# Performance work log

Measured on AMD Instinct MI355X. Metric: run time of the kernel, lower is better.

Reference implementation:

```python
import jax, jax.numpy as jnp
import numpy as np

# Constants matching init_kwargs
FEATURE_DIM = 512
QK_DIM = 128
GATE_VALUE = 0.2
TOPK = 32
TEMP = QK_DIM ** (-0.5)


def _l2norm(x, eps=1e-12):
    # F.normalize(p=2, dim=-1): x / max(||x||_2, eps)
    return x / jnp.maximum(jnp.linalg.norm(x, axis=-1, keepdims=True), eps)


def setup_inputs() -> dict:
    key = jax.random.key(0)
    ks = jax.random.split(key, 6)
    B, Nq, Nk = 64, 512, 2048  # Nq == FEATURE_DIM (required by the gather/residual shapes)
    query = jax.random.normal(ks[0], (B, Nq, FEATURE_DIM), dtype=jnp.float32)
    key_feat = jax.random.normal(ks[1], (B, Nk, FEATURE_DIM // 2), dtype=jnp.float32)
    value = jax.random.normal(ks[2], (B, Nk, FEATURE_DIM // 2), dtype=jnp.float32)
    # torch.nn.Linear weights are [out, in]; init N(0, sqrt(2/out_features))
    WQ = jax.random.normal(ks[3], (QK_DIM, FEATURE_DIM), dtype=jnp.float32) * np.sqrt(2.0 / QK_DIM).astype(np.float32)
    WK = jax.random.normal(ks[4], (QK_DIM, FEATURE_DIM // 2), dtype=jnp.float32) * np.sqrt(2.0 / QK_DIM).astype(np.float32)
    WV = jax.random.normal(ks[5], (FEATURE_DIM, FEATURE_DIM // 2), dtype=jnp.float32) * np.sqrt(2.0 / FEATURE_DIM).astype(np.float32)
    return {"query": query, "key_feat": key_feat, "value": value, "WQ": WQ, "WK": WK, "WV": WV}


def reference(query, key_feat, value, WQ, WK, WV):
    # Projections (Linear, no bias) + L2 normalize
    w_q = _l2norm(jnp.einsum('bqf,df->bqd', query, WQ))        # [B, Nq, Dqk]
    w_k = _l2norm(jnp.einsum('bkf,df->bkd', key_feat, WK))     # [B, Nk, Dqk]
    dot_prod = jnp.einsum('bqd,bkd->bqk', w_q, w_k)            # [B, Nq, Nk]
    mask = jnp.max(dot_prod, axis=2) > GATE_VALUE              # [B, Nq] bool
    affinity = jax.nn.softmax(dot_prod * TEMP, axis=-1)        # [B, Nq, Nk]
    topk_vals, topk_idx = jax.lax.top_k(affinity, TOPK)        # [B, Nq, TOPK]
    w_v = _l2norm(jnp.einsum('bkf,cf->bkc', value, WV))        # [B, Nk, F]
    # Faithful torch.gather semantics: index permuted to [B, TOPK, Nq];
    # sel[b,t,c] = w_v[b, topk_idx[b,c,t], c]  (per-channel gather, needs Nq == F)
    sel = jnp.take_along_axis(w_v, jnp.swapaxes(topk_idx, 1, 2), axis=1)  # [B, TOPK, F]
    gather = jnp.einsum('bqt,btc->bqc', topk_vals, sel)        # [B, Nq, F]
    return gather * mask[:, :, None].astype(gather.dtype) + query
```

## Files before the change

### kernel.cpp

```cpp
#include <hip/hip_runtime.h>
#include <math.h>

#define NB   64
#define NQ   512
#define NK   2048
#define FD   512
#define FH   256
#define DQ   128
#define KTOP 32
#define GATEV 0.2f
#define TEMPF 0.08838834764831843f
#define GATEY 0.017677669529663688f

typedef __attribute__((ext_vector_type(8))) short bf16x8;
typedef __attribute__((ext_vector_type(4))) float f32x4;

__device__ __forceinline__ unsigned short f32_bf16_rne(float f) {
    unsigned u = __float_as_uint(f);
    u += 0x7FFFu + ((u >> 16) & 1u);
    return (unsigned short)(u >> 16);
}
__device__ __forceinline__ float exp_small(float y) {
    return 1.f + y * (1.f + y * (0.5f + y * (0.16666667f + y * 0.041666668f)));
}
__device__ __forceinline__ unsigned f32_ordkey(float y, unsigned idc) {
    unsigned bits = __float_as_uint(y);
    unsigned msk = (unsigned)((int)bits >> 31) | 0x80000000u;
    return ((bits ^ msk) & 0xFFFFF800u) | idc;
}
__device__ __forceinline__ float keyval_f(unsigned key) {
    unsigned x = key & 0xFFFFF800u;
    unsigned bits = (x & 0x80000000u) ? (x ^ 0x80000000u) : ~x;
    return __uint_as_float(bits);
}
__device__ __forceinline__ bf16x8 cvt8(const float* p) {
    float4 a = ((const float4*)p)[0];
    float4 b = ((const float4*)p)[1];
    bf16x8 o;
    o[0] = (short)f32_bf16_rne(a.x); o[1] = (short)f32_bf16_rne(a.y);
    o[2] = (short)f32_bf16_rne(a.z); o[3] = (short)f32_bf16_rne(a.w);
    o[4] = (short)f32_bf16_rne(b.x); o[5] = (short)f32_bf16_rne(b.y);
    o[6] = (short)f32_bf16_rne(b.z); o[7] = (short)f32_bf16_rne(b.w);
    return o;
}
__device__ __forceinline__ unsigned umaxu(unsigned a, unsigned b) { return a > b ? a : b; }
__device__ __forceinline__ unsigned uminu(unsigned a, unsigned b) { return a < b ? a : b; }

__global__ __launch_bounds__(256) void kW_cvt(const float* __restrict__ WQ,
                                              const float* __restrict__ WK,
                                              const float* __restrict__ WV,
                                              unsigned short* __restrict__ wqW,
                                              unsigned short* __restrict__ wkW,
                                              unsigned short* __restrict__ wvb) {
    const int i = blockIdx.x * 256 + threadIdx.x;
    if (i < 65536) wqW[i] = f32_bf16_rne(WQ[i]);
    else if (i < 98304) wkW[i - 65536] = f32_bf16_rne(WK[i - 65536]);
    else wvb[i - 98304] = f32_bf16_rne(WV[i - 98304]);
}

__global__ __launch_bounds__(256) void kProjQ(const float* __restrict__ X,
                                              const unsigned short* __restrict__ Wb,
                                              unsigned short* __restrict__ outb) {
    __shared__ __attribute__((aligned(16))) unsigned short wchunk[64 * 512];
    const int tid = threadIdx.x, wave = tid >> 6, lane = tid & 63;
    const int rt = lane & 15, kg = lane >> 4;
    const size_t rowbase = (size_t)blockIdx.x * 64 + wave * 16;
    const float* xrow = X + (rowbase + rt) * 512;
    bf16x8 afr[16];
#pragma unroll
    for (int s = 0; s < 16; ++s) afr[s] = cvt8(xrow + kg * 8 + s * 32);
    f32x4 acc[8];
#pragma unroll
    for (int j = 0; j < 8; ++j) acc[j] = (f32x4){0.f, 0.f, 0.f, 0.f};
#pragma unroll
    for (int ch = 0; ch < 2; ++ch) {
        __syncthreads();
#pragma unroll
        for (int it = 0; it < 16; ++it) {
            int idx = it * 256 + tid;
            int cl = idx >> 6, g = idx & 63;
            *(bf16x8*)(wchunk + (cl * 64 + (g ^ (cl & 7))) * 8) =
                *(const bf16x8*)(Wb + (size_t)(ch * 64 + cl) * 512 + g * 8);
        }
        __syncthreads();
#pragma unroll 1
        for (int ct = 0; ct < 4; ++ct) {
            const int cl = ct * 16 + rt;
            const int jg = ch * 4 + ct;
#pragma unroll
            for (int s = 0; s < 16; ++s) {
                int gr = cl * 64 + ((s * 4 + kg) ^ (cl & 7));
                bf16x8 bfr = *(const bf16x8*)(wchunk + gr * 8);
                acc[jg] = __builtin_amdgcn_mfma_f32_16x16x32_bf16(afr[s], bfr, acc[jg], 0, 0, 0);
            }
        }
    }
    float nrm[4];
#pragma unroll
    for (int r = 0; r < 4; ++r) {
        float s = 0.f;
#pragma unroll
        for (int j = 0; j < 8; ++j) s += acc[j][r] * acc[j][r];
        nrm[r] = s;
    }
#pragma unroll
    for (int o = 1; o < 16; o <<= 1) {
#pragma unroll
        for (int r = 0; r < 4; ++r) nrm[r] += __shfl_xor(nrm[r], o);
    }
    float inv[4];
#pragma unroll
    for (int r = 0; r < 4; ++r) inv[r] = 1.f / fmaxf(sqrtf(nrm[r]), 1e-12f);
#pragma unroll
    for (int j = 0; j < 8; ++j) {
#pragma unroll
        for (int r = 0; r < 4; ++r)
            outb[(rowbase + kg * 4 + r) * DQ + j * 16 + rt] = f32_bf16_rne(acc[j][r] * inv[r]);
    }
}

__global__ __launch_bounds__(256) void kProjK(const float* __restrict__ X,
                                              const unsigned short* __restrict__ Wb,
                                              unsigned short* __restrict__ outb,
                                              float* __restrict__ invk) {
    __shared__ __attribute__((aligned(16))) unsigned short wchunk[128 * 256];
    const int tid = threadIdx.x, wave = tid >> 6, lane = tid & 63;
    const int rt = lane & 15, kg = lane >> 4;
    const size_t rowbase = (size_t)blockIdx.x * 128 + wave * 32;

    bf16x8 afr[2][8];
#pragma unroll
    for (int m = 0; m < 2; ++m) {
        const float* xrow = X + (rowbase + m * 16 + rt) * 256;
#pragma unroll
        for (int s = 0; s < 8; ++s) afr[m][s] = cvt8(xrow + kg * 8 + s * 32);
    }
#pragma unroll
    for (int it = 0; it < 16; ++it) {
        int idx = it * 256 + tid;
        int cl = idx >> 5, g = idx & 31;
        *(bf16x8*)(wchunk + (cl * 32 + (g ^ (cl & 7))) * 8) =
            *(const bf16x8*)(Wb + (size_t)cl * 256 + g * 8);
    }
    __syncthreads();

    float nrm[2][4] = {{0.f,0.f,0.f,0.f},{0.f,0.f,0.f,0.f}};
#pragma unroll 1
    for (int ct = 0; ct < 8; ++ct) {
        const int cl = ct * 16 + rt;
#pragma unroll
        for (int m = 0; m < 2; ++m) {
            f32x4 acc = {0.f, 0.f, 0.f, 0.f};
#pragma unroll
            for (int s = 0; s < 8; ++s) {
                int gr = cl * 32 + ((s * 4 + kg) ^ (cl & 7));
                bf16x8 bfr = *(const bf16x8*)(wchunk + gr * 8);
                acc = __builtin_amdgcn_mfma_f32_16x16x32_bf16(afr[m][s], bfr, acc, 0, 0, 0);
            }
#pragma unroll
            for (int r = 0; r < 4; ++r) {
                outb[(rowbase + m * 16 + kg * 4 + r) * DQ + ct * 16 + rt] = f32_bf16_rne(acc[r]);
                nrm[m][r] += acc[r] * acc[r];
            }
        }
    }
#pragma unroll
    for (int o = 1; o < 16; o <<= 1) {
#pragma unroll
        for (int m = 0; m < 2; ++m)
#pragma unroll
            for (int r = 0; r < 4; ++r) nrm[m][r] += __shfl_xor(nrm[m][r], o);
    }
    if (rt == 0) {
#pragma unroll
        for (int m = 0; m < 2; ++m)
#pragma unroll
            for (int r = 0; r < 4; ++r)
                invk[rowbase + m * 16 + kg * 4 + r] = 1.f / fmaxf(sqrtf(nrm[m][r]), 1e-12f);
    }
}

__global__ __launch_bounds__(256) void kC2_vnorm(const float* __restrict__ value,
                                                 const unsigned short* __restrict__ wvb,
                                                 float* __restrict__ invnv) {
    __shared__ __attribute__((aligned(16))) unsigned short wchunk[128 * 256];
    const int tid = threadIdx.x, wave = tid >> 6, lane = tid & 63;
    const int rt = lane & 15, kg = lane >> 4;
    const size_t rowbase = (size_t)blockIdx.x * 128 + wave * 32;

    bf16x8 afr[2][8];
#pragma unroll
    for (int m = 0; m < 2; ++m) {
        const float* vrow = value + (rowbase + m * 16 + rt) * FH;
#pragma unroll
        for (int s = 0; s < 8; ++s) afr[m][s] = cvt8(vrow + kg * 8 + s * 32);
    }
    float nrm[2][4] = {{0.f,0.f,0.f,0.f},{0.f,0.f,0.f,0.f}};

    for (int ch = 0; ch < 4; ++ch) {
        __syncthreads();
        const unsigned short* src = wvb + (size_t)ch * 128 * FH;
#pragma unroll
        for (int it = 0; it < 16; ++it) {
            int idx = it * 256 + tid;
            int c_local = idx >> 5, g = idx & 31;
            int dst = c_local * 32 + (g ^ (c_local & 7));
            *(bf16x8*)(wchunk + dst * 8) = *(const bf16x8*)(src + (size_t)c_local * FH + g * 8);
        }
        __syncthreads();
#pragma unroll 1
        for (int ct = 0; ct < 8; ++ct) {
            const int cl = ct * 16 + rt;
            f32x4 acc0 = {0.f,0.f,0.f,0.f}, acc1 = {0.f,0.f,0.f,0.f};
#pragma unroll
            for (int s = 0; s < 8; ++s) {
                int gr = cl * 32 + ((s * 4 + kg) ^ (cl & 7));
                bf16x8 bfr = *(const bf16x8*)(wchunk + gr * 8);
                acc0 = __builtin_amdgcn_mfma_f32_16x16x32_bf16(afr[0][s], bfr, acc0, 0, 0, 0);
                acc1 = __builtin_amdgcn_mfma_f32_16x16x32_bf16(afr[1][s], bfr, acc1, 0, 0, 0);
            }
#pragma unroll
            for (int r = 0; r < 4; ++r) {
                nrm[0][r] += acc0[r] * acc0[r];
                nrm[1][r] += acc1[r] * acc1[r];
            }
        }
    }
#pragma unroll
    for (int o = 1; o < 16; o <<= 1) {
#pragma unroll
        for (int m = 0; m < 2; ++m)
#pragma unroll
            for (int r = 0; r < 4; ++r) nrm[m][r] += __shfl_xor(nrm[m][r], o);
    }
    if (rt == 0) {
#pragma unroll
        for (int m = 0; m < 2; ++m)
#pragma unroll
            for (int r = 0; r < 4; ++r)
                invnv[rowbase + m * 16 + kg * 4 + r] = 1.f / fmaxf(sqrtf(nrm[m][r]), 1e-12f);
    }
}

__global__ __launch_bounds__(512) void kD_fused(const unsigned short* __restrict__ wqb,
                                                const unsigned short* __restrict__ wkb,
                                                const float* __restrict__ invk,
                                                float* __restrict__ vals,
                                                int* __restrict__ idxs,
                                                float* __restrict__ maskf) {
    __shared__ unsigned cand[64][128];
    __shared__ float sums1[64][8];
    __shared__ float sums2[64][8];
    const int tid = threadIdx.x, wave = tid >> 6, lane = tid & 63;
    const int rt = lane & 15, kg = lane >> 4;
    const int wid = (blockIdx.x & 7) * 64 + (blockIdx.x >> 3);
    const int b = wid >> 3;
    const size_t qrow0 = (size_t)b * NQ + (wid & 7) * 64;

    bf16x8 afr[4][4];
#pragma unroll
    for (int m = 0; m < 4; ++m) {
        const unsigned short* aq = wqb + (qrow0 + m * 16 + rt) * DQ + kg * 8;
#pragma unroll
        for (int s = 0; s < 4; ++s) afr[m][s] = *(const bf16x8*)(aq + s * 32);
    }

    const unsigned short* bk0 = wkb + ((size_t)b * NK + wave * 256 + rt) * DQ + kg * 8;
    const float* ivp = invk + (size_t)b * NK + wave * 256 + rt;
    unsigned best[4][4];
    float s1[4][4], s2[4][4];
#pragma unroll
    for (int m = 0; m < 4; ++m)
#pragma unroll
        for (int r = 0; r < 4; ++r) { best[m][r] = 0u; s1[m][r] = 0.f; s2[m][r] = 0.f; }

#pragma unroll 2
    for (int kt = 0; kt < 16; ++kt) {
        const unsigned short* bk = bk0 + (size_t)kt * 16 * DQ;
        bf16x8 bfr[4];
#pragma unroll
        for (int s = 0; s < 4; ++s) bfr[s] = *(const bf16x8*)(bk + s * 32);
        const unsigned idc = 2047u - (unsigned)(wave * 256 + kt * 16 + rt);
        const float ivT = ivp[kt * 16] * TEMPF;
#pragma unroll
        for (int m = 0; m < 4; ++m) {
            f32x4 acc = {0.f, 0.f, 0.f, 0.f};
#pragma unroll
            for (int s = 0; s < 4; ++s)
                acc = __builtin_amdgcn_mfma_f32_16x16x32_bf16(afr[m][s], bfr[s], acc, 0, 0, 0);
#pragma unroll
            for (int r = 0; r < 4; ++r) {
                const float y = acc[r] * ivT;
                best[m][r] = umaxu(best[m][r], f32_ordkey(y, idc));
                s1[m][r] += y;
                s2[m][r] = fmaf(y, y, s2[m][r]);
            }
        }
    }
#pragma unroll
    for (int o = 1; o < 16; o <<= 1) {
#pragma unroll
        for (int m = 0; m < 4; ++m)
#pragma unroll
            for (int r = 0; r < 4; ++r) {
                s1[m][r] += __shfl_xor(s1[m][r], o);
                s2[m][r] += __shfl_xor(s2[m][r], o);
            }
    }
#pragma unroll
    for (int m = 0; m < 4; ++m)
#pragma unroll
        for (int r = 0; r < 4; ++r) cand[m * 16 + kg * 4 + r][wave * 16 + rt] = best[m][r];
    if (rt == 0) {
#pragma unroll
        for (int m = 0; m < 4; ++m)
#pragma unroll
            for (int r = 0; r < 4; ++r) {
                sums1[m * 16 + kg * 4 + r][wave] = s1[m][r];
                sums2[m * 16 + kg * 4 + r][wave] = s2[m][r];
            }
    }
    __syncthreads();

#pragma unroll 1
    for (int rr = 0; rr < 8; ++rr) {
        const int row = wave * 8 + rr;
        float S1 = sums1[row][lane & 7], S2 = sums2[row][lane & 7];
#pragma unroll
        for (int o = 1; o < 8; o <<= 1) { S1 += __shfl_xor(S1, o); S2 += __shfl_xor(S2, o); }
        const float invA = 1.f / (2048.f + S1 + 0.5f * S2);

        unsigned c0 = umaxu(cand[row][lane], cand[row][lane + 64]);
#pragma unroll
        for (int kq = 2; kq <= 64; kq <<= 1) {
#pragma unroll
            for (int jj = kq >> 1; jj > 0; jj >>= 1) {
                unsigned x0 = __shfl_xor(c0, jj);
                const bool keepmax = (((lane & jj) == 0) ^ ((lane & kq) != 0));
                c0 = keepmax ? umaxu(c0, x0) : uminu(c0, x0);
            }
        }
        const float maxy = keyval_f(__shfl((int)c0, 0));
        if (lane == 0) maskf[qrow0 + row] = (maxy > GATEY) ? 1.f : 0.f;
        if (lane < KTOP) {
            const size_t gr0 = (qrow0 + row) * KTOP;
            vals[gr0 + lane] = exp_small(keyval_f(c0)) * invA;
            idxs[gr0 + lane] = (int)(2047u - (c0 & 0x7FFu));
        }
    }
}

__global__ __launch_bounds__(256) void kE_sel(const float* __restrict__ value,
                                              const float* __restrict__ WV,
                                              const float* __restrict__ invnv,
                                              const int* __restrict__ idxs,
                                              unsigned short* __restrict__ selT) {
    __shared__ __attribute__((aligned(16))) float wvc[FH];
    __shared__ int id_s[KTOP];
    const int tid = threadIdx.x;
    const int wid = (blockIdx.x & 7) * 4096 + (blockIdx.x >> 3);
    const int b = wid >> 9;
    const int c = wid & 511;
    wvc[tid] = WV[(size_t)c * FH + tid];
    if (tid < KTOP) id_s[tid] = idxs[((size_t)b * NQ + c) * KTOP + tid];
    __syncthreads();
    const int t = tid >> 3;
    const int l8 = tid & 7;
    const int k = id_s[t];
    const float4* v4 = (const float4*)(value + ((size_t)b * NK + k) * FH);
    const float4* w4 = (const float4*)wvc;
    float s = 0.f;
#pragma unroll
    for (int m = 0; m < 8; ++m) {
        float4 a = v4[l8 + 8 * m];
        float4 w = w4[l8 + 8 * m];
        s += a.x * w.x + a.y * w.y + a.z * w.z + a.w * w.w;
    }
#pragma unroll
    for (int o = 4; o > 0; o >>= 1) s += __shfl_down(s, o, 8);
    if (l8 == 0)
        selT[((size_t)b * FD + c) * KTOP + t] = f32_bf16_rne(s * invnv[(size_t)b * NK + k]);
}

__global__ __launch_bounds__(256) void kF_out(const float* __restrict__ vals,
                                              const unsigned short* __restrict__ selT,
                                              const float* __restrict__ maskf,
                                              const float* __restrict__ query,
                                              float* __restrict__ out) {
    const int tid = threadIdx.x, wave = tid >> 6, lane = tid & 63;
    const int rt = lane & 15, kg = lane >> 4;
    const int b = blockIdx.x >> 5;
    const int q0 = (blockIdx.x & 31) * 16;
    const int cbase = wave * 128;

    bf16x8 afr = cvt8(vals + ((size_t)b * NQ + q0 + rt) * KTOP + kg * 8);
    f32x4 acc[8];
#pragma unroll
    for (int ct = 0; ct < 8; ++ct) {
        bf16x8 bfr = *(const bf16x8*)(selT + ((size_t)b * FD + cbase + ct * 16 + rt) * KTOP + kg * 8);
        acc[ct] = __builtin_amdgcn_mfma_f32_16x16x32_bf16(afr, bfr, (f32x4){0.f,0.f,0.f,0.f}, 0, 0, 0);
    }
    float m[4];
#pragma unroll
    for (int r = 0; r < 4; ++r) m[r] = maskf[(size_t)b * NQ + q0 + kg * 4 + r];
#pragma unroll
    for (int ct = 0; ct < 8; ++ct) {
#pragma unroll
        for (int r = 0; r < 4; ++r) {
            const size_t off = ((size_t)b * NQ + q0 + kg * 4 + r) * FD + cbase + ct * 16 + rt;
            out[off] = fmaf(m[r], acc[ct][r], query[off]);
        }
    }
}

extern "C" void kernel_launch(void* const* d_in, const int* in_sizes, int n_in,
                              void* d_out, int out_size, void* d_ws, size_t ws_size,
                              hipStream_t stream) {
    (void)in_sizes; (void)n_in; (void)out_size; (void)ws_size;
    const float* query = (const float*)d_in[0];
    const float* keyf  = (const float*)d_in[1];
    const float* value = (const float*)d_in[2];
    const float* WQ    = (const float*)d_in[3];
    const float* WK    = (const float*)d_in[4];
    const float* WV    = (const float*)d_in[5];
    float* out = (float*)d_out;

    unsigned short* wqb = (unsigned short*)d_ws;
    unsigned short* wkb = wqb + (size_t)NB * NQ * DQ;
    unsigned short* wvb = wkb + (size_t)NB * NK * DQ;
    unsigned short* wqW = wvb + (size_t)FD * FH;
    unsigned short* wkW = wqW + (size_t)DQ * FD;
    float* invnv = (float*)(wkW + (size_t)DQ * FH);
    float* invk  = invnv + (size_t)NB * NK;
    float* vals  = invk + (size_t)NB * NK;
    int*   idxs  = (int*)(vals + (size_t)NB * NQ * KTOP);
    float* maskf = (float*)(idxs + (size_t)NB * NQ * KTOP);
    unsigned short* selT = (unsigned short*)(maskf + (size_t)NB * NQ);

    kW_cvt<<<dim3(896), dim3(256), 0, stream>>>(WQ, WK, WV, wqW, wkW, wvb);
    kProjQ<<<dim3(NB * NQ / 64), dim3(256), 0, stream>>>(query, wqW, wqb);
    kProjK<<<dim3(NB * NK / 128), dim3(256), 0, stream>>>(keyf, wkW, wkb, invk);
    kC2_vnorm<<<dim3(NB * NK / 128), dim3(256), 0, stream>>>(value, wvb, invnv);
    kD_fused<<<dim3(512), dim3(512), 0, stream>>>(wqb, wkb, invk, vals, idxs, maskf);
    kE_sel<<<dim3(NB * FD), dim3(256), 0, stream>>>(value, WV, invnv, idxs, selT);
    kF_out<<<dim3(NB * 32), dim3(256), 0, stream>>>(vals, selT, maskf, query, out);
}
```

Measured before the change: 278.6 us.

## Pre-swizzle weights into MFMA fragment order and read B operands directly from global

The weight conversion kernel now writes WQ, WK and WV in bf16 already arranged in the per-lane MFMA B-fragment order, with each thread converting 8 elements. The three projection kernels drop their shared-memory weight staging and barriers and load B fragments straight from global or L2 with coalesced 16-byte loads. This removes LDS traffic, the __syncthreads calls and the LDS footprint, which may allow more blocks per CU. The trade-off is that every wave re-fetches weights through the cache hierarchy instead of sharing one LDS copy per block.

Result: slower. 331.3 us (+18.9%).

```diff
diff --git a/kernel.cpp b/kernel.cpp
--- a/kernel.cpp
+++ b/kernel.cpp
@@ -49,19 +49,36 @@
 __global__ __launch_bounds__(256) void kW_cvt(const float* __restrict__ WQ,
                                               const float* __restrict__ WK,
                                               const float* __restrict__ WV,
-                                              unsigned short* __restrict__ wqW,
-                                              unsigned short* __restrict__ wkW,
-                                              unsigned short* __restrict__ wvb) {
-    const int i = blockIdx.x * 256 + threadIdx.x;
-    if (i < 65536) wqW[i] = f32_bf16_rne(WQ[i]);
-    else if (i < 98304) wkW[i - 65536] = f32_bf16_rne(WK[i - 65536]);
-    else wvb[i - 98304] = f32_bf16_rne(WV[i - 98304]);
+                                              unsigned short* __restrict__ wqF,
+                                              unsigned short* __restrict__ wkF,
+                                              unsigned short* __restrict__ wvF) {
+    const int t = blockIdx.x * 256 + threadIdx.x;
+    if (t < 8192) {
+        int fidx = t >> 6, lane = t & 63;
+        int ct = fidx >> 4, s = fidx & 15;
+        int rt = lane & 15, kg = lane >> 4;
+        *(bf16x8*)(wqF + (size_t)t * 8) =
+            cvt8(WQ + (size_t)(ct * 16 + rt) * 512 + (s * 4 + kg) * 8);
+    } else if (t < 12288) {
+        int u = t - 8192;
+        int fidx = u >> 6, lane = u & 63;
+        int ct = fidx >> 3, s = fidx & 7;
+        int rt = lane & 15, kg = lane >> 4;
+        *(bf16x8*)(wkF + (size_t)u * 8) =
+            cvt8(WK + (size_t)(ct * 16 + rt) * 256 + (s * 4 + kg) * 8);
+    } else {
+        int u = t - 12288;
+        int fidx = u >> 6, lane = u & 63;
+        int ct = fidx >> 3, s = fidx & 7;
+        int rt = lane & 15, kg = lane >> 4;
+        *(bf16x8*)(wvF + (size_t)u * 8) =
+            cvt8(WV + (size_t)(ct * 16 + rt) * 256 + (s * 4 + kg) * 8);
+    }
 }
 
 __global__ __launch_bounds__(256) void kProjQ(const float* __restrict__ X,
-                                              const unsigned short* __restrict__ Wb,
+                                              const unsigned short* __restrict__ wqF,
                                               unsigned short* __restrict__ outb) {
-    __shared__ __attribute__((aligned(16))) unsigned short wchunk[64 * 512];
     const int tid = threadIdx.x, wave = tid >> 6, lane = tid & 63;
     const int rt = lane & 15, kg = lane >> 4;
     const size_t rowbase = (size_t)blockIdx.x * 64 + wave * 16;
@@ -72,28 +89,15 @@
     f32x4 acc[8];
 #pragma unroll
     for (int j = 0; j < 8; ++j) acc[j] = (f32x4){0.f, 0.f, 0.f, 0.f};
-#pragma unroll
-    for (int ch = 0; ch < 2; ++ch) {
-        __syncthreads();
-#pragma unroll
-        for (int it = 0; it < 16; ++it) {
-            int idx = it * 256 + tid;
-            int cl = idx >> 6, g = idx & 63;
-            *(bf16x8*)(wchunk + (cl * 64 + (g ^ (cl & 7))) * 8) =
-                *(const bf16x8*)(Wb + (size_t)(ch * 64 + cl) * 512 + g * 8);
-        }
-        __syncthreads();
 #pragma unroll 1
-        for (int ct = 0; ct < 4; ++ct) {
-            const int cl = ct * 16 + rt;
-            const int jg = ch * 4 + ct;
-#pragma unroll
-            for (int s = 0; s < 16; ++s) {
-                int gr = cl * 64 + ((s * 4 + kg) ^ (cl & 7));
-                bf16x8 bfr = *(const bf16x8*)(wchunk + gr * 8);
-                acc[jg] = __builtin_amdgcn_mfma_f32_16x16x32_bf16(afr[s], bfr, acc[jg], 0, 0, 0);
-            }
-        }
+    for (int ct = 0; ct < 8; ++ct) {
+        f32x4 a = acc[ct];
+#pragma unroll
+        for (int s = 0; s < 16; ++s) {
+            bf16x8 bfr = *(const bf16x8*)(wqF + ((size_t)(ct * 16 + s) * 64 + lane) * 8);
+            a = __builtin_amdgcn_mfma_f32_16x16x32_bf16(afr[s], bfr, a, 0, 0, 0);
+        }
+        acc[ct] = a;
     }
     float nrm[4];
 #pragma unroll
@@ -120,10 +124,9 @@
 }
 
 __global__ __launch_bounds__(256) void kProjK(const float* __restrict__ X,
-                                              const unsigned short* __restrict__ Wb,
+                                              const unsigned short* __restrict__ wkF,
                                               unsigned short* __restrict__ outb,
                                               float* __restrict__ invk) {
-    __shared__ __attribute__((aligned(16))) unsigned short wchunk[128 * 256];
     const int tid = threadIdx.x, wave = tid >> 6, lane = tid & 63;
     const int rt = lane & 15, kg = lane >> 4;
     const size_t rowbase = (size_t)blockIdx.x * 128 + wave * 32;
@@ -135,26 +138,15 @@
 #pragma unroll
         for (int s = 0; s < 8; ++s) afr[m][s] = cvt8(xrow + kg * 8 + s * 32);
     }
-#pragma unroll
-    for (int it = 0; it < 16; ++it) {
-        int idx = it * 256 + tid;
-        int cl = idx >> 5, g = idx & 31;
-        *(bf16x8*)(wchunk + (cl * 32 + (g ^ (cl & 7))) * 8) =
-            *(const bf16x8*)(Wb + (size_t)cl * 256 + g * 8);
-    }
-    __syncthreads();
-
     float nrm[2][4] = {{0.f,0.f,0.f,0.f},{0.f,0.f,0.f,0.f}};
 #pragma unroll 1
     for (int ct = 0; ct < 8; ++ct) {
-        const int cl = ct * 16 + rt;
 #pragma unroll
         for (int m = 0; m < 2; ++m) {
             f32x4 acc = {0.f, 0.f, 0.f, 0.f};
 #pragma unroll
             for (int s = 0; s < 8; ++s) {
-                int gr = cl * 32 + ((s * 4 + kg) ^ (cl & 7));
-                bf16x8 bfr = *(const bf16x8*)(wchunk + gr * 8);
+                bf16x8 bfr = *(const bf16x8*)(wkF + ((size_t)(ct * 8 + s) * 64 + lane) * 8);
                 acc = __builtin_amdgcn_mfma_f32_16x16x32_bf16(afr[m][s], bfr, acc, 0, 0, 0);
             }
 #pragma unroll
@@ -181,9 +173,8 @@
 }
 
 __global__ __launch_bounds__(256) void kC2_vnorm(const float* __restrict__ value,
-                                                 const unsigned short* __restrict__ wvb,
+                                                 const unsigned short* __restrict__ wvF,
                                                  float* __restrict__ invnv) {
-    __shared__ __attribute__((aligned(16))) unsigned short wchunk[128 * 256];
     const int tid = threadIdx.x, wave = tid >> 6, lane = tid & 63;
     const int rt = lane & 15, kg = lane >> 4;
     const size_t rowbase = (size_t)blockIdx.x * 128 + wave * 32;
@@ -196,34 +187,19 @@
         for (int s = 0; s < 8; ++s) afr[m][s] = cvt8(vrow + kg * 8 + s * 32);
     }
     float nrm[2][4] = {{0.f,0.f,0.f,0.f},{0.f,0.f,0.f,0.f}};
-
-    for (int ch = 0; ch < 4; ++ch) {
-        __syncthreads();
-        const unsigned short* src = wvb + (size_t)ch * 128 * FH;
-#pragma unroll
-        for (int it = 0; it < 16; ++it) {
-            int idx = it * 256 + tid;
-            int c_local = idx >> 5, g = idx & 31;
-            int dst = c_local * 32 + (g ^ (c_local & 7));
-            *(bf16x8*)(wchunk + dst * 8) = *(const bf16x8*)(src + (size_t)c_local * FH + g * 8);
-        }
-        __syncthreads();
-#pragma unroll 1
-        for (int ct = 0; ct < 8; ++ct) {
-            const int cl = ct * 16 + rt;
-            f32x4 acc0 = {0.f,0.f,0.f,0.f}, acc1 = {0.f,0.f,0.f,0.f};
-#pragma unroll
-            for (int s = 0; s < 8; ++s) {
-                int gr = cl * 32 + ((s * 4 + kg) ^ (cl & 7));
-                bf16x8 bfr = *(const bf16x8*)(wchunk + gr * 8);
-                acc0 = __builtin_amdgcn_mfma_f32_16x16x32_bf16(afr[0][s], bfr, acc0, 0, 0, 0);
-                acc1 = __builtin_amdgcn_mfma_f32_16x16x32_bf16(afr[1][s], bfr, acc1, 0, 0, 0);
-            }
-#pragma unroll
-            for (int r = 0; r < 4; ++r) {
-                nrm[0][r] += acc0[r] * acc0[r];
-                nrm[1][r] += acc1[r] * acc1[r];
-            }
+#pragma unroll 2
+    for (int ct = 0; ct < 32; ++ct) {
+        f32x4 acc0 = {0.f,0.f,0.f,0.f}, acc1 = {0.f,0.f,0.f,0.f};
+#pragma unroll
+        for (int s = 0; s < 8; ++s) {
+            bf16x8 bfr = *(const bf16x8*)(wvF + ((size_t)(ct * 8 + s) * 64 + lane) * 8);
+            acc0 = __builtin_amdgcn_mfma_f32_16x16x32_bf16(afr[0][s], bfr, acc0, 0, 0, 0);
+            acc1 = __builtin_amdgcn_mfma_f32_16x16x32_bf16(afr[1][s], bfr, acc1, 0, 0, 0);
+        }
+#pragma unroll
+        for (int r = 0; r < 4; ++r) {
+            nrm[0][r] += acc0[r] * acc0[r];
+            nrm[1][r] += acc1[r] * acc1[r];
         }
     }
 #pragma unroll
@@ -427,20 +403,20 @@
 
     unsigned short* wqb = (unsigned short*)d_ws;
     unsigned short* wkb = wqb + (size_t)NB * NQ * DQ;
-    unsigned short* wvb = wkb + (size_t)NB * NK * DQ;
-    unsigned short* wqW = wvb + (size_t)FD * FH;
-    unsigned short* wkW = wqW + (size_t)DQ * FD;
-    float* invnv = (float*)(wkW + (size_t)DQ * FH);
+    unsigned short* wvF = wkb + (size_t)NB * NK * DQ;
+    unsigned short* wqF = wvF + (size_t)FD * FH;
+    unsigned short* wkF = wqF + (size_t)DQ * FD;
+    float* invnv = (float*)(wkF + (size_t)DQ * FH);
     float* invk  = invnv + (size_t)NB * NK;
     float* vals  = invk + (size_t)NB * NK;
     int*   idxs  = (int*)(vals + (size_t)NB * NQ * KTOP);
     float* maskf = (float*)(idxs + (size_t)NB * NQ * KTOP);
     unsigned short* selT = (unsigned short*)(maskf + (size_t)NB * NQ);
 
-    kW_cvt<<<dim3(896), dim3(256), 0, stream>>>(WQ, WK, WV, wqW, wkW, wvb);
-    kProjQ<<<dim3(NB * NQ / 64), dim3(256), 0, stream>>>(query, wqW, wqb);
-    kProjK<<<dim3(NB * NK / 128), dim3(256), 0, stream>>>(keyf, wkW, wkb, invk);
-    kC2_vnorm<<<dim3(NB * NK / 128), dim3(256), 0, stream>>>(value, wvb, invnv);
+    kW_cvt<<<dim3(112), dim3(256), 0, stream>>>(WQ, WK, WV, wqF, wkF, wvF);
+    kProjQ<<<dim3(NB * NQ / 64), dim3(256), 0, stream>>>(query, wqF, wqb);
+    kProjK<<<dim3(NB * NK / 128), dim3(256), 0, stream>>>(keyf, wkF, wkb, invk);
+    kC2_vnorm<<<dim3(NB * NK / 128), dim3(256), 0, stream>>>(value, wvF, invnv);
     kD_fused<<<dim3(512), dim3(512), 0, stream>>>(wqb, wkb, invk, vals, idxs, maskf);
     kE_sel<<<dim3(NB * FD), dim3(256), 0, stream>>>(value, WV, invnv, idxs, selT);
     kF_out<<<dim3(NB * 32), dim3(256), 0, stream>>>(vals, selT, maskf, query, out);
```
